# Kernel optimization log

Measured on AMD Instinct MI355X. Metric: run time of the kernel, lower is better.

Reference implementation:

```python
import jax, jax.numpy as jnp
import numpy as np
import math

N, E, B, T = 100000, 500000, 4096, 12
IN, HID, H = 64, 32, 4
HC = HID * H  # 128
ED = 4


def setup_inputs() -> dict:
    key = jax.random.key(0)
    ks = jax.random.split(key, 40)
    w = lambda k, shape: jax.random.normal(k, shape, jnp.float32) * 0.05
    inp = {
        'x': jax.random.normal(ks[0], (N, IN), jnp.float32),
        'edge_index': jax.random.randint(ks[1], (2, E), 0, N, jnp.int32),
        'edge_attr': jax.random.normal(ks[2], (E, ED), jnp.float32),
        'batch': jnp.sort(jax.random.randint(ks[3], (N,), 0, B, jnp.int32)),
        'r_target': jax.random.randint(ks[4], (B,), 0, T, jnp.int32),
        # layer 1 (in=IN)
        'Wq1': w(ks[5], (IN, HC)), 'bq1': w(ks[6], (HC,)),
        'Wk1': w(ks[7], (IN, HC)), 'bk1': w(ks[8], (HC,)),
        'Wv1': w(ks[9], (IN, HC)), 'bv1': w(ks[10], (HC,)),
        'We1': w(ks[11], (ED, HC)),
        'Ws1': w(ks[12], (IN, HC)), 'bs1': w(ks[13], (HC,)),
        # layers 2 and 3 stacked (in=HC)
        'Wq23': w(ks[14], (2, HC, HC)), 'bq23': w(ks[15], (2, HC)),
        'Wk23': w(ks[16], (2, HC, HC)), 'bk23': w(ks[17], (2, HC)),
        'Wv23': w(ks[18], (2, HC, HC)), 'bv23': w(ks[19], (2, HC)),
        'We23': w(ks[20], (2, ED, HC)),
        'Ws23': w(ks[21], (2, HC, HC)), 'bs23': w(ks[22], (2, HC)),
        # per-task linear heads (out_channels=1)
        'head_W': w(ks[23], (T, HC)), 'head_b': w(ks[24], (T,)),
    }
    return inp


def tconv(x, src, dst, ea, Wq, bq, Wk, bk, Wv, bv, We, Ws, bs):
    """PyG TransformerConv: gather -> per-edge MHA score -> segment softmax -> scatter."""
    q = (x @ Wq + bq).reshape(-1, H, HID)   # [N,H,C]
    k = (x @ Wk + bk).reshape(-1, H, HID)
    v = (x @ Wv + bv).reshape(-1, H, HID)
    e = (ea @ We).reshape(-1, H, HID)       # [E,H,C] (lin_edge has no bias)
    kj = k[src] + e                          # [E,H,C]
    alpha = (q[dst] * kj).sum(-1) / math.sqrt(HID)          # [E,H]
    amax = jax.ops.segment_max(alpha, dst, num_segments=N)  # [N,H]
    alpha = jnp.exp(alpha - amax[dst])
    asum = jax.ops.segment_sum(alpha, dst, num_segments=N)
    alpha = alpha / (asum[dst] + 1e-16)
    msg = (v[src] + e) * alpha[..., None]                   # [E,H,C]
    out = jax.ops.segment_sum(msg, dst, num_segments=N).reshape(N, HC)
    return out + x @ Ws + bs                 # root_weight skip connection


def reference(x, edge_index, edge_attr, batch, r_target,
              Wq1, bq1, Wk1, bk1, Wv1, bv1, We1, Ws1, bs1,
              Wq23, bq23, Wk23, bk23, Wv23, bv23, We23, Ws23, bs23,
              head_W, head_b):
    src, dst = edge_index[0], edge_index[1]
    h = jax.nn.relu(tconv(x, src, dst, edge_attr, Wq1, bq1, Wk1, bk1, Wv1, bv1, We1, Ws1, bs1))
    h = jax.nn.relu(tconv(h, src, dst, edge_attr, Wq23[0], bq23[0], Wk23[0], bk23[0], Wv23[0], bv23[0], We23[0], Ws23[0], bs23[0]))
    h = tconv(h, src, dst, edge_attr, Wq23[1], bq23[1], Wk23[1], bk23[1], Wv23[1], bv23[1], We23[1], Ws23[1], bs23[1])
    # global mean pool per graph
    cnt = jax.ops.segment_sum(jnp.ones((N,), h.dtype), batch, num_segments=B)
    pooled = jax.ops.segment_sum(h, batch, num_segments=B) / jnp.maximum(cnt, 1.0)[:, None]  # [B,HC]
    # dropout p=0.3 is a no-op in eval mode
    # per-task head selected by r_target (out_channels=1, squeezed)
    return (pooled * head_W[r_target]).sum(-1) + head_b[r_target]  # [B]
```

## Files before the change

kernel.cpp:

```cpp
#include <hip/hip_runtime.h>
#include <hip/hip_bf16.h>

#define NN 100000
#define EE 500000
#define BB 4096
#define HC 128
#define SCAN_ELEM 1024
#define NSB ((NN + SCAN_ELEM - 1) / SCAN_ELEM)

typedef __bf16 bf16_t;
typedef bf16_t bf16x8 __attribute__((ext_vector_type(8)));
typedef float f32x4 __attribute__((ext_vector_type(4)));

__device__ __forceinline__ unsigned short f2bf(float f) {
    unsigned u = __builtin_bit_cast(unsigned, f);
    u += 0x7FFFu + ((u >> 16) & 1u);
    return (unsigned short)(u >> 16);
}
__device__ __forceinline__ float bflo(unsigned u) {
    return __builtin_bit_cast(float, u << 16);
}
__device__ __forceinline__ float bfhi(unsigned u) {
    return __builtin_bit_cast(float, u & 0xFFFF0000u);
}

__global__ __launch_bounds__(256) void conv_x(const float* __restrict__ in,
                                              unsigned short* __restrict__ outb,
                                              int total4)
{
    const int g = blockIdx.x * 256 + threadIdx.x;
    if (g >= total4) return;
    const float4 f = *(const float4*)(in + (size_t)g * 4);
    ushort4 u;
    u.x = f2bf(f.x); u.y = f2bf(f.y); u.z = f2bf(f.z); u.w = f2bf(f.w);
    *(ushort4*)(outb + (size_t)g * 4) = u;
}

__global__ __launch_bounds__(256) void prep_w(
    const float* __restrict__ Wq, const float* __restrict__ Wk,
    const float* __restrict__ Wv, const float* __restrict__ Ws,
    unsigned short* __restrict__ Wt, int K)
{
    const int g = blockIdx.x * 256 + threadIdx.x;
    const int per = K * 128;
    if (g >= 4 * per) return;
    const int p = g / per, r = g - p * per;
    const int k = r >> 7, n = r & 127;
    const float* W = p == 0 ? Wq : p == 1 ? Wk : p == 2 ? Wv : Ws;
    Wt[(size_t)p * per + (size_t)n * K + k] = f2bf(W[k * 128 + n]);
}

template<int NKT>
__global__ __launch_bounds__(256) void gemm_mfma(
    const unsigned short* __restrict__ A,
    const unsigned short* __restrict__ Wt,
    const float* __restrict__ bq, const float* __restrict__ bk,
    const float* __restrict__ bv, const float* __restrict__ bs,
    unsigned* __restrict__ Qb, unsigned* __restrict__ Kb,
    unsigned* __restrict__ Vb, float* __restrict__ S)
{
    constexpr int K = NKT * 32;
    const int lane = threadIdx.x & 63;
    const int p = threadIdx.x >> 6;
    const int m = lane & 15, kq = lane >> 4;
    const int rows0 = blockIdx.x * 32;

    const unsigned short* Wp = Wt + (size_t)p * 128 * K;
    const float* bias = p == 0 ? bq : p == 1 ? bk : p == 2 ? bv : bs;

    bf16x8 a[2][NKT];
#pragma unroll
    for (int mt = 0; mt < 2; mt++)
#pragma unroll
        for (int kt = 0; kt < NKT; kt++)
            a[mt][kt] = *(const bf16x8*)(A + (size_t)(rows0 + mt * 16 + m) * K + kt * 32 + kq * 8);

    f32x4 acc[2][8];
#pragma unroll
    for (int mt = 0; mt < 2; mt++)
#pragma unroll
        for (int nt = 0; nt < 8; nt++)
            acc[mt][nt] = (f32x4){0.f, 0.f, 0.f, 0.f};

#pragma unroll
    for (int nt = 0; nt < 8; nt++) {
#pragma unroll
        for (int kt = 0; kt < NKT; kt++) {
            const bf16x8 b = *(const bf16x8*)(Wp + (size_t)(nt * 16 + m) * K + kt * 32 + kq * 8);
            acc[0][nt] = __builtin_amdgcn_mfma_f32_16x16x32_bf16(a[0][kt], b, acc[0][nt], 0, 0, 0);
            acc[1][nt] = __builtin_amdgcn_mfma_f32_16x16x32_bf16(a[1][kt], b, acc[1][nt], 0, 0, 0);
        }
    }

    if (p == 3) {
#pragma unroll
        for (int nt = 0; nt < 8; nt++) {
            const float bi = bias[nt * 16 + m];
#pragma unroll
            for (int mt = 0; mt < 2; mt++) {
                float* o = S + (size_t)(rows0 + mt * 16 + kq * 4) * HC + nt * 16 + m;
#pragma unroll
                for (int r = 0; r < 4; r++) o[r * HC] = acc[mt][nt][r] + bi;
            }
        }
    } else {
        unsigned* out = p == 0 ? Qb : p == 1 ? Kb : Vb;
#pragma unroll
        for (int nt = 0; nt < 8; nt++) {
            const float bi = bias[nt * 16 + m];
#pragma unroll
            for (int mt = 0; mt < 2; mt++) {
#pragma unroll
                for (int r = 0; r < 4; r++) {
                    const float v0 = acc[mt][nt][r] + bi;
                    const float v1 = __shfl_xor(v0, 1);
                    if (!(m & 1)) {
                        const unsigned pk = (unsigned)f2bf(v0) | ((unsigned)f2bf(v1) << 16);
                        out[(size_t)(rows0 + mt * 16 + kq * 4 + r) * 64 + nt * 8 + (m >> 1)] = pk;
                    }
                }
            }
        }
    }
}

__global__ __launch_bounds__(256) void deg_k(const int* __restrict__ ei, int* __restrict__ deg)
{
    const int e = blockIdx.x * 256 + threadIdx.x;
    if (e < EE) atomicAdd(&deg[ei[EE + e]], 1);
}

__global__ __launch_bounds__(256) void scan_part(const int* __restrict__ deg,
                                                 int* __restrict__ bsum)
{
    __shared__ int red[256];
    const int base = blockIdx.x * SCAN_ELEM + threadIdx.x * 4;
    int s = 0;
#pragma unroll
    for (int j = 0; j < 4; j++) { const int i = base + j; if (i < NN) s += deg[i]; }
    red[threadIdx.x] = s;
    __syncthreads();
    for (int st = 128; st > 0; st >>= 1) {
        if (threadIdx.x < st) red[threadIdx.x] += red[threadIdx.x + st];
        __syncthreads();
    }
    if (threadIdx.x == 0) bsum[blockIdx.x] = red[0];
}

__global__ __launch_bounds__(128) void scan_top(const int* __restrict__ bsum,
                                                int* __restrict__ boff)
{
    __shared__ int buf[128];
    const int v = (threadIdx.x < NSB) ? bsum[threadIdx.x] : 0;
    buf[threadIdx.x] = v;
    __syncthreads();
    for (int s = 1; s < 128; s <<= 1) {
        const int t = (threadIdx.x >= s) ? buf[threadIdx.x - s] : 0;
        __syncthreads();
        buf[threadIdx.x] += t;
        __syncthreads();
    }
    if (threadIdx.x < NSB) boff[threadIdx.x] = buf[threadIdx.x] - v;
}

__global__ __launch_bounds__(256) void scan_final(const int* __restrict__ deg,
                                                  const int* __restrict__ boff,
                                                  int* __restrict__ off,
                                                  int* __restrict__ cursor)
{
    __shared__ int tsum[256];
    const int base = blockIdx.x * SCAN_ELEM + threadIdx.x * 4;
    int vals[4];
    int s = 0;
#pragma unroll
    for (int j = 0; j < 4; j++) {
        const int i = base + j;
        vals[j] = (i < NN) ? deg[i] : 0;
        s += vals[j];
    }
    tsum[threadIdx.x] = s;
    __syncthreads();
    for (int st = 1; st < 256; st <<= 1) {
        const int t = (threadIdx.x >= st) ? tsum[threadIdx.x - st] : 0;
        __syncthreads();
        tsum[threadIdx.x] += t;
        __syncthreads();
    }
    int ex = boff[blockIdx.x] + tsum[threadIdx.x] - s;
#pragma unroll
    for (int j = 0; j < 4; j++) {
        const int i = base + j;
        if (i < NN) { off[i] = ex; cursor[i] = ex; }
        ex += vals[j];
    }
    if (blockIdx.x == NSB - 1 && threadIdx.x == 255)
        off[NN] = boff[blockIdx.x] + tsum[255];
}

__global__ __launch_bounds__(256) void bucket_k(const int* __restrict__ ei,
                                                const float* __restrict__ ea,
                                                int* __restrict__ cursor,
                                                int* __restrict__ esrc,
                                                float4* __restrict__ eaf)
{
    const int e = blockIdx.x * 256 + threadIdx.x;
    if (e < EE) {
        const int d = ei[EE + e];
        const int p = atomicAdd(&cursor[d], 1);
        esrc[p] = ei[e];
        eaf[p] = *(const float4*)(ea + (size_t)e * 4);
    }
}

__global__ __launch_bounds__(256) void cnt_k(const int* __restrict__ batch,
                                             float* __restrict__ cnt)
{
    const int n = blockIdx.x * 256 + threadIdx.x;
    if (n < NN) atomicAdd(&cnt[batch[n]], 1.0f);
}

__global__ __launch_bounds__(256) void edge_fused(
    const int* __restrict__ esrc, const float4* __restrict__ eaf,
    const float* __restrict__ We,
    const unsigned* __restrict__ Qb, const unsigned* __restrict__ Kb,
    const unsigned* __restrict__ Vb,
    const int* __restrict__ off, const float* __restrict__ S,
    unsigned short* __restrict__ Hb,
    const int* __restrict__ batch, float* __restrict__ pooled,
    int fuse_pool)
{
    __shared__ float wes[512];
    for (int i = threadIdx.x; i < 512; i += 256) wes[i] = We[i];
    __syncthreads();

    const int lane = threadIdx.x & 63;
    const int n = blockIdx.x * 4 + (threadIdx.x >> 6);
    const int c = lane * 2;
    const float w00 = wes[c],     w10 = wes[128 + c],     w20 = wes[256 + c],     w30 = wes[384 + c];
    const float w01 = wes[c + 1], w11 = wes[128 + c + 1], w21 = wes[256 + c + 1], w31 = wes[384 + c + 1];

    const int beg = off[n], end = off[n + 1];
    const unsigned qu = Qb[(size_t)n * 64 + lane];
    const float q0 = bflo(qu), q1 = bfhi(qu);
    float num0 = 0.f, num1 = 0.f, den = 0.f;

    int src = 0;
    float4 a4 = make_float4(0.f, 0.f, 0.f, 0.f);
    if (beg < end) { src = esrc[beg]; a4 = eaf[beg]; }

    for (int p = beg; p < end; p++) {
        const unsigned ku = Kb[(size_t)src * 64 + lane];
        const unsigned vu = Vb[(size_t)src * 64 + lane];
        const float4 ac = a4;
        if (p + 1 < end) { src = esrc[p + 1]; a4 = eaf[p + 1]; }
        const float e0 = ac.x * w00 + ac.y * w10 + ac.z * w20 + ac.w * w30;
        const float e1 = ac.x * w01 + ac.y * w11 + ac.z * w21 + ac.w * w31;
        float part = q0 * (bflo(ku) + e0) + q1 * (bfhi(ku) + e1);
        part += __shfl_xor(part, 1);
        part += __shfl_xor(part, 2);
        part += __shfl_xor(part, 4);
        part += __shfl_xor(part, 8);
        const float al = expf(part * 0.17677669529663687f);
        num0 += (bflo(vu) + e0) * al;
        num1 += (bfhi(vu) + e1) * al;
        den += al;
    }

    const float2 skip = *(const float2*)(S + (size_t)n * HC + c);
    const float inv = 1.f / (den + 1e-16f);
    float o0 = num0 * inv + skip.x;
    float o1 = num1 * inv + skip.y;
    if (!fuse_pool) {
        o0 = fmaxf(o0, 0.f);
        o1 = fmaxf(o1, 0.f);
        const unsigned pk = (unsigned)f2bf(o0) | ((unsigned)f2bf(o1) << 16);
        *(unsigned*)(Hb + (size_t)n * HC + c) = pk;
    } else {
        const int b = batch[n];
        atomicAdd(pooled + (size_t)b * HC + c, o0);
        atomicAdd(pooled + (size_t)b * HC + c + 1, o1);
    }
}

__global__ __launch_bounds__(256) void head_k(
    const float* __restrict__ pooled, const float* __restrict__ cnt,
    const int* __restrict__ rt, const float* __restrict__ hW,
    const float* __restrict__ hb, float* __restrict__ out)
{
    const int lane = threadIdx.x & 63;
    const int b = blockIdx.x * 4 + (threadIdx.x >> 6);
    if (b >= BB) return;
    const int t = rt[b];
    const int c = lane * 2;
    const float2 p2 = *(const float2*)(pooled + (size_t)b * HC + c);
    const float2 w2 = *(const float2*)(hW + (size_t)t * HC + c);
    float part = p2.x * w2.x + p2.y * w2.y;
    part += __shfl_xor(part, 1);
    part += __shfl_xor(part, 2);
    part += __shfl_xor(part, 4);
    part += __shfl_xor(part, 8);
    part += __shfl_xor(part, 16);
    part += __shfl_xor(part, 32);
    if (lane == 0) out[b] = part / fmaxf(cnt[b], 1.0f) + hb[t];
}

extern "C" void kernel_launch(void* const* d_in, const int* in_sizes, int n_in,
                              void* d_out, int out_size, void* d_ws, size_t ws_size,
                              hipStream_t stream) {
    const float* x      = (const float*)d_in[0];
    const int*   ei     = (const int*)d_in[1];
    const float* ea     = (const float*)d_in[2];
    const int*   batch  = (const int*)d_in[3];
    const int*   rt     = (const int*)d_in[4];

    float* ws     = (float*)d_ws;
    float* Hbuf   = ws;
    unsigned* Qb  = (unsigned*)(ws + 12800000);
    unsigned* Kb  = Qb + 6400000;
    unsigned* Vb  = Kb + 6400000;
    unsigned short* Abf = (unsigned short*)(Vb + 6400000);
    float4* eaf   = (float4*)(Abf + 12800000);
    unsigned short* Wt = (unsigned short*)(eaf + 500000);
    float* pooled = (float*)(Wt + 65536);
    float* cnt    = pooled + 524288;
    int*   esrc   = (int*)(cnt + 4096);
    int*   deg    = esrc + 500000;
    int*   off    = deg + 100000;
    int*   cursor = off + 100004;
    int*   bsum   = cursor + 100000;
    int*   boff   = bsum + 128;

    hipMemsetAsync(deg, 0, 100000 * sizeof(int), stream);
    deg_k<<<(EE + 255) / 256, 256, 0, stream>>>(ei, deg);
    scan_part<<<NSB, 256, 0, stream>>>(deg, bsum);
    scan_top<<<1, 128, 0, stream>>>(bsum, boff);
    scan_final<<<NSB, 256, 0, stream>>>(deg, boff, off, cursor);
    bucket_k<<<(EE + 255) / 256, 256, 0, stream>>>(ei, ea, cursor, esrc, eaf);

    hipMemsetAsync(pooled, 0, (size_t)(BB * HC + BB) * sizeof(float), stream);
    cnt_k<<<(NN + 255) / 256, 256, 0, stream>>>(batch, cnt);

    conv_x<<<(NN * 64 / 4 + 255) / 256, 256, 0, stream>>>(x, Abf, NN * 64 / 4);

    for (int l = 0; l < 3; l++) {
        const int K = (l == 0) ? 64 : 128;
        const float *Wq, *Wk, *Wv, *Wsk, *bq, *bk, *bv, *bs, *We;
        if (l == 0) {
            Wq = (const float*)d_in[5];  bq = (const float*)d_in[6];
            Wk = (const float*)d_in[7];  bk = (const float*)d_in[8];
            Wv = (const float*)d_in[9];  bv = (const float*)d_in[10];
            We = (const float*)d_in[11];
            Wsk= (const float*)d_in[12]; bs = (const float*)d_in[13];
        } else {
            const int j = l - 1;
            Wq = (const float*)d_in[14] + (size_t)j * HC * HC;  bq = (const float*)d_in[15] + j * HC;
            Wk = (const float*)d_in[16] + (size_t)j * HC * HC;  bk = (const float*)d_in[17] + j * HC;
            Wv = (const float*)d_in[18] + (size_t)j * HC * HC;  bv = (const float*)d_in[19] + j * HC;
            We = (const float*)d_in[20] + (size_t)j * 4 * HC;
            Wsk= (const float*)d_in[21] + (size_t)j * HC * HC;  bs = (const float*)d_in[22] + j * HC;
        }

        prep_w<<<(4 * K * 128 + 255) / 256, 256, 0, stream>>>(Wq, Wk, Wv, Wsk, Wt, K);
        if (K == 64)
            gemm_mfma<2><<<NN / 32, 256, 0, stream>>>(Abf, Wt, bq, bk, bv, bs, Qb, Kb, Vb, Hbuf);
        else
            gemm_mfma<4><<<NN / 32, 256, 0, stream>>>(Abf, Wt, bq, bk, bv, bs, Qb, Kb, Vb, Hbuf);
        edge_fused<<<NN / 4, 256, 0, stream>>>(esrc, eaf, We, Qb, Kb, Vb, off,
                                               Hbuf, Abf, batch, pooled,
                                               l == 2 ? 1 : 0);
    }

    head_k<<<BB / 4, 256, 0, stream>>>(pooled, cnt, rt,
        (const float*)d_in[23], (const float*)d_in[24], (float*)d_out);
}
```

Baseline: 665.9 us.

## Process four edges per wavefront in parallel with 16-byte feature loads

New measurement: 653.9 us. About the same (-1.8%).

```diff
diff --git a/kernel.cpp b/kernel.cpp
--- a/kernel.cpp
+++ b/kernel.cpp
@@ -229,56 +229,107 @@
     const int* __restrict__ batch, float* __restrict__ pooled,
     int fuse_pool)
 {
-    __shared__ float wes[512];
-    for (int i = threadIdx.x; i < 512; i += 256) wes[i] = We[i];
-    __syncthreads();
-
     const int lane = threadIdx.x & 63;
+    const int slot = lane >> 4;
+    const int c8   = lane & 15;
     const int n = blockIdx.x * 4 + (threadIdx.x >> 6);
-    const int c = lane * 2;
-    const float w00 = wes[c],     w10 = wes[128 + c],     w20 = wes[256 + c],     w30 = wes[384 + c];
-    const float w01 = wes[c + 1], w11 = wes[128 + c + 1], w21 = wes[256 + c + 1], w31 = wes[384 + c + 1];
+
+    float w[4][8];
+#pragma unroll
+    for (int d = 0; d < 4; d++) {
+        const float4 a = *(const float4*)(We + d * HC + c8 * 8);
+        const float4 b = *(const float4*)(We + d * HC + c8 * 8 + 4);
+        w[d][0] = a.x; w[d][1] = a.y; w[d][2] = a.z; w[d][3] = a.w;
+        w[d][4] = b.x; w[d][5] = b.y; w[d][6] = b.z; w[d][7] = b.w;
+    }
+
+    const uint4 qv = *(const uint4*)(Qb + (size_t)n * 64 + c8 * 4);
+    float q[8];
+    q[0] = bflo(qv.x); q[1] = bfhi(qv.x); q[2] = bflo(qv.y); q[3] = bfhi(qv.y);
+    q[4] = bflo(qv.z); q[5] = bfhi(qv.z); q[6] = bflo(qv.w); q[7] = bfhi(qv.w);
 
     const int beg = off[n], end = off[n + 1];
-    const unsigned qu = Qb[(size_t)n * 64 + lane];
-    const float q0 = bflo(qu), q1 = bfhi(qu);
-    float num0 = 0.f, num1 = 0.f, den = 0.f;
-
-    int src = 0;
-    float4 a4 = make_float4(0.f, 0.f, 0.f, 0.f);
-    if (beg < end) { src = esrc[beg]; a4 = eaf[beg]; }
-
-    for (int p = beg; p < end; p++) {
-        const unsigned ku = Kb[(size_t)src * 64 + lane];
-        const unsigned vu = Vb[(size_t)src * 64 + lane];
-        const float4 ac = a4;
-        if (p + 1 < end) { src = esrc[p + 1]; a4 = eaf[p + 1]; }
-        const float e0 = ac.x * w00 + ac.y * w10 + ac.z * w20 + ac.w * w30;
-        const float e1 = ac.x * w01 + ac.y * w11 + ac.z * w21 + ac.w * w31;
-        float part = q0 * (bflo(ku) + e0) + q1 * (bfhi(ku) + e1);
-        part += __shfl_xor(part, 1);
-        part += __shfl_xor(part, 2);
-        part += __shfl_xor(part, 4);
-        part += __shfl_xor(part, 8);
-        const float al = expf(part * 0.17677669529663687f);
-        num0 += (bflo(vu) + e0) * al;
-        num1 += (bfhi(vu) + e1) * al;
-        den += al;
-    }
-
-    const float2 skip = *(const float2*)(S + (size_t)n * HC + c);
+    float num[8] = {0.f, 0.f, 0.f, 0.f, 0.f, 0.f, 0.f, 0.f};
+    float den = 0.f;
+
+    if (beg < end) {
+        int p0 = beg + slot; if (p0 >= end) p0 = end - 1;
+        int src = esrc[p0];
+        float4 a4 = eaf[p0];
+        for (int base = beg; base < end; base += 4) {
+            const bool act = (base + slot) < end;
+            const uint4 ku = *(const uint4*)(Kb + (size_t)src * 64 + c8 * 4);
+            const uint4 vu = *(const uint4*)(Vb + (size_t)src * 64 + c8 * 4);
+            const float4 ac = a4;
+            if (base + 4 < end) {
+                int pn = base + 4 + slot; if (pn >= end) pn = end - 1;
+                src = esrc[pn];
+                a4 = eaf[pn];
+            }
+            float e[8];
+#pragma unroll
+            for (int j = 0; j < 8; j++)
+                e[j] = ac.x * w[0][j] + ac.y * w[1][j] + ac.z * w[2][j] + ac.w * w[3][j];
+            float part = q[0] * (bflo(ku.x) + e[0]) + q[1] * (bfhi(ku.x) + e[1])
+                       + q[2] * (bflo(ku.y) + e[2]) + q[3] * (bfhi(ku.y) + e[3])
+                       + q[4] * (bflo(ku.z) + e[4]) + q[5] * (bfhi(ku.z) + e[5])
+                       + q[6] * (bflo(ku.w) + e[6]) + q[7] * (bfhi(ku.w) + e[7]);
+            part += __shfl_xor(part, 1);
+            part += __shfl_xor(part, 2);
+            float al = __expf(part * 0.17677669529663687f);
+            if (!act) al = 0.f;
+            num[0] += (bflo(vu.x) + e[0]) * al;
+            num[1] += (bfhi(vu.x) + e[1]) * al;
+            num[2] += (bflo(vu.y) + e[2]) * al;
+            num[3] += (bfhi(vu.y) + e[3]) * al;
+            num[4] += (bflo(vu.z) + e[4]) * al;
+            num[5] += (bfhi(vu.z) + e[5]) * al;
+            num[6] += (bflo(vu.w) + e[6]) * al;
+            num[7] += (bfhi(vu.w) + e[7]) * al;
+            den += al;
+        }
+    }
+
+#pragma unroll
+    for (int j = 0; j < 8; j++) {
+        num[j] += __shfl_xor(num[j], 16);
+        num[j] += __shfl_xor(num[j], 32);
+    }
+    den += __shfl_xor(den, 16);
+    den += __shfl_xor(den, 32);
     const float inv = 1.f / (den + 1e-16f);
-    float o0 = num0 * inv + skip.x;
-    float o1 = num1 * inv + skip.y;
+
     if (!fuse_pool) {
-        o0 = fmaxf(o0, 0.f);
-        o1 = fmaxf(o1, 0.f);
-        const unsigned pk = (unsigned)f2bf(o0) | ((unsigned)f2bf(o1) << 16);
-        *(unsigned*)(Hb + (size_t)n * HC + c) = pk;
+        if (slot == 0) {
+            const float4 s0 = *(const float4*)(S + (size_t)n * HC + c8 * 8);
+            const float4 s1 = *(const float4*)(S + (size_t)n * HC + c8 * 8 + 4);
+            float o[8];
+            o[0] = fmaxf(num[0] * inv + s0.x, 0.f);
+            o[1] = fmaxf(num[1] * inv + s0.y, 0.f);
+            o[2] = fmaxf(num[2] * inv + s0.z, 0.f);
+            o[3] = fmaxf(num[3] * inv + s0.w, 0.f);
+            o[4] = fmaxf(num[4] * inv + s1.x, 0.f);
+            o[5] = fmaxf(num[5] * inv + s1.y, 0.f);
+            o[6] = fmaxf(num[6] * inv + s1.z, 0.f);
+            o[7] = fmaxf(num[7] * inv + s1.w, 0.f);
+            uint4 pk;
+            pk.x = (unsigned)f2bf(o[0]) | ((unsigned)f2bf(o[1]) << 16);
+            pk.y = (unsigned)f2bf(o[2]) | ((unsigned)f2bf(o[3]) << 16);
+            pk.z = (unsigned)f2bf(o[4]) | ((unsigned)f2bf(o[5]) << 16);
+            pk.w = (unsigned)f2bf(o[6]) | ((unsigned)f2bf(o[7]) << 16);
+            *(uint4*)(Hb + (size_t)n * HC + c8 * 8) = pk;
+        }
     } else {
+        float oe, oo;
+        if      (slot == 0) { oe = num[0]; oo = num[1]; }
+        else if (slot == 1) { oe = num[2]; oo = num[3]; }
+        else if (slot == 2) { oe = num[4]; oo = num[5]; }
+        else                { oe = num[6]; oo = num[7]; }
+        const int c = c8 * 8 + slot * 2;
+        const float2 s2 = *(const float2*)(S + (size_t)n * HC + c);
         const int b = batch[n];
-        atomicAdd(pooled + (size_t)b * HC + c, o0);
-        atomicAdd(pooled + (size_t)b * HC + c + 1, o1);
+        atomicAdd(pooled + (size_t)b * HC + c,     oe * inv + s2.x);
+        atomicAdd(pooled + (size_t)b * HC + c + 1, oo * inv + s2.y);
     }
 }
 
```

## Process four edges per wave with interleaved K/V rows and factored edge terms

Applied to the files above, without the earlier changes.

Result: no change. 670.3 us (+0.7%).

```diff
diff --git a/kernel.cpp b/kernel.cpp
--- a/kernel.cpp
+++ b/kernel.cpp
@@ -11,6 +11,7 @@
 typedef __bf16 bf16_t;
 typedef bf16_t bf16x8 __attribute__((ext_vector_type(8)));
 typedef float f32x4 __attribute__((ext_vector_type(4)));
+typedef float f32x2 __attribute__((ext_vector_type(2)));
 
 __device__ __forceinline__ unsigned short f2bf(float f) {
     unsigned u = __builtin_bit_cast(unsigned, f);
@@ -22,6 +23,9 @@
 }
 __device__ __forceinline__ float bfhi(unsigned u) {
     return __builtin_bit_cast(float, u & 0xFFFF0000u);
+}
+__device__ __forceinline__ f32x2 unpk2(unsigned u) {
+    return (f32x2){ bflo(u), bfhi(u) };
 }
 
 __global__ __launch_bounds__(256) void conv_x(const float* __restrict__ in,
@@ -56,8 +60,8 @@
     const unsigned short* __restrict__ Wt,
     const float* __restrict__ bq, const float* __restrict__ bk,
     const float* __restrict__ bv, const float* __restrict__ bs,
-    unsigned* __restrict__ Qb, unsigned* __restrict__ Kb,
-    unsigned* __restrict__ Vb, float* __restrict__ S)
+    unsigned* __restrict__ Qb, unsigned* __restrict__ KVb,
+    float* __restrict__ S)
 {
     constexpr int K = NKT * 32;
     const int lane = threadIdx.x & 63;
@@ -104,7 +108,8 @@
             }
         }
     } else {
-        unsigned* out = p == 0 ? Qb : p == 1 ? Kb : Vb;
+        unsigned* out = p == 0 ? Qb : (p == 1 ? KVb : KVb + 64);
+        const int stride = p == 0 ? 64 : 128;
 #pragma unroll
         for (int nt = 0; nt < 8; nt++) {
             const float bi = bias[nt * 16 + m];
@@ -116,7 +121,7 @@
                     const float v1 = __shfl_xor(v0, 1);
                     if (!(m & 1)) {
                         const unsigned pk = (unsigned)f2bf(v0) | ((unsigned)f2bf(v1) << 16);
-                        out[(size_t)(rows0 + mt * 16 + kq * 4 + r) * 64 + nt * 8 + (m >> 1)] = pk;
+                        out[(size_t)(rows0 + mt * 16 + kq * 4 + r) * stride + nt * 8 + (m >> 1)] = pk;
                     }
                 }
             }
@@ -222,63 +227,135 @@
 __global__ __launch_bounds__(256) void edge_fused(
     const int* __restrict__ esrc, const float4* __restrict__ eaf,
     const float* __restrict__ We,
-    const unsigned* __restrict__ Qb, const unsigned* __restrict__ Kb,
-    const unsigned* __restrict__ Vb,
+    const unsigned* __restrict__ Qb, const unsigned* __restrict__ KVb,
     const int* __restrict__ off, const float* __restrict__ S,
     unsigned short* __restrict__ Hb,
     const int* __restrict__ batch, float* __restrict__ pooled,
     int fuse_pool)
 {
-    __shared__ float wes[512];
-    for (int i = threadIdx.x; i < 512; i += 256) wes[i] = We[i];
-    __syncthreads();
-
     const int lane = threadIdx.x & 63;
+    const int slot = lane >> 4;
+    const int c8   = lane & 15;
+    const int cb   = c8 * 8;
+    const int ceq  = cb + slot * 2;
     const int n = blockIdx.x * 4 + (threadIdx.x >> 6);
-    const int c = lane * 2;
-    const float w00 = wes[c],     w10 = wes[128 + c],     w20 = wes[256 + c],     w30 = wes[384 + c];
-    const float w01 = wes[c + 1], w11 = wes[128 + c + 1], w21 = wes[256 + c + 1], w31 = wes[384 + c + 1];
 
     const int beg = off[n], end = off[n + 1];
-    const unsigned qu = Qb[(size_t)n * 64 + lane];
-    const float q0 = bflo(qu), q1 = bfhi(qu);
-    float num0 = 0.f, num1 = 0.f, den = 0.f;
-
-    int src = 0;
-    float4 a4 = make_float4(0.f, 0.f, 0.f, 0.f);
-    if (beg < end) { src = esrc[beg]; a4 = eaf[beg]; }
-
-    for (int p = beg; p < end; p++) {
-        const unsigned ku = Kb[(size_t)src * 64 + lane];
-        const unsigned vu = Vb[(size_t)src * 64 + lane];
-        const float4 ac = a4;
-        if (p + 1 < end) { src = esrc[p + 1]; a4 = eaf[p + 1]; }
-        const float e0 = ac.x * w00 + ac.y * w10 + ac.z * w20 + ac.w * w30;
-        const float e1 = ac.x * w01 + ac.y * w11 + ac.z * w21 + ac.w * w31;
-        float part = q0 * (bflo(ku) + e0) + q1 * (bfhi(ku) + e1);
-        part += __shfl_xor(part, 1);
-        part += __shfl_xor(part, 2);
-        part += __shfl_xor(part, 4);
-        part += __shfl_xor(part, 8);
-        const float al = expf(part * 0.17677669529663687f);
-        num0 += (bflo(vu) + e0) * al;
-        num1 += (bfhi(vu) + e1) * al;
+
+    const float2 sk2 = *(const float2*)(S + (size_t)n * HC + ceq);
+    const uint4 qv = *(const uint4*)(Qb + (size_t)n * 64 + c8 * 4);
+    f32x2 q2[4];
+    q2[0] = unpk2(qv.x); q2[1] = unpk2(qv.y);
+    q2[2] = unpk2(qv.z); q2[3] = unpk2(qv.w);
+
+    float qep[4];
+#pragma unroll
+    for (int d = 0; d < 4; d++) {
+        const float4 wa = *(const float4*)(We + d * HC + cb);
+        const float4 wb = *(const float4*)(We + d * HC + cb + 4);
+        qep[d] = wa.x * q2[0].x + wa.y * q2[0].y + wa.z * q2[1].x + wa.w * q2[1].y
+               + wb.x * q2[2].x + wb.y * q2[2].y + wb.z * q2[3].x + wb.w * q2[3].y;
+    }
+
+    f32x2 num2[4] = {(f32x2){0.f, 0.f}, (f32x2){0.f, 0.f},
+                     (f32x2){0.f, 0.f}, (f32x2){0.f, 0.f}};
+    f32x4 s4 = (f32x4){0.f, 0.f, 0.f, 0.f};
+    float den = 0.f;
+
+    auto COMPUTE = [&](const uint4& ku, const uint4& vu, const float4& ac, bool act) {
+        f32x2 t2 = q2[0] * unpk2(ku.x);
+        t2 += q2[1] * unpk2(ku.y);
+        t2 += q2[2] * unpk2(ku.z);
+        t2 += q2[3] * unpk2(ku.w);
+        float tot = t2.x + t2.y
+                  + ac.x * qep[0] + ac.y * qep[1] + ac.z * qep[2] + ac.w * qep[3];
+        tot += __shfl_xor(tot, 1);
+        tot += __shfl_xor(tot, 2);
+        float al = __expf(tot * 0.17677669529663687f);
+        if (!act) al = 0.f;
+        num2[0] += unpk2(vu.x) * al;
+        num2[1] += unpk2(vu.y) * al;
+        num2[2] += unpk2(vu.z) * al;
+        num2[3] += unpk2(vu.w) * al;
+        s4.x += ac.x * al; s4.y += ac.y * al;
+        s4.z += ac.z * al; s4.w += ac.w * al;
         den += al;
-    }
-
-    const float2 skip = *(const float2*)(S + (size_t)n * HC + c);
+    };
+
+    if (beg < end) {
+        const int e1 = end - 1;
+        int p0 = beg + slot; if (p0 > e1) p0 = e1;
+        const int srcA = esrc[p0];
+        const float4 aA = eaf[p0];
+        const unsigned* kvA = KVb + (size_t)srcA * 128 + c8 * 4;
+        const uint4 kA = *(const uint4*)kvA;
+        const uint4 vA = *(const uint4*)(kvA + 64);
+        if (beg + 4 < end) {
+            int p1 = beg + 4 + slot; if (p1 > e1) p1 = e1;
+            const int srcB = esrc[p1];
+            float4 aB = eaf[p1];
+            const unsigned* kvB = KVb + (size_t)srcB * 128 + c8 * 4;
+            uint4 kB = *(const uint4*)kvB;
+            uint4 vB = *(const uint4*)(kvB + 64);
+            COMPUTE(kA, vA, aA, true);
+            int base = beg + 4;
+            for (;;) {
+                if (base + 4 < end) {
+                    int pn = base + 4 + slot; if (pn > e1) pn = e1;
+                    const int srcN = esrc[pn];
+                    const float4 aN = eaf[pn];
+                    COMPUTE(kB, vB, aB, (base + slot) < end);
+                    const unsigned* kvN = KVb + (size_t)srcN * 128 + c8 * 4;
+                    kB = *(const uint4*)kvN;
+                    vB = *(const uint4*)(kvN + 64);
+                    aB = aN;
+                    base += 4;
+                } else {
+                    COMPUTE(kB, vB, aB, (base + slot) < end);
+                    break;
+                }
+            }
+        } else {
+            COMPUTE(kA, vA, aA, (beg + slot) < end);
+        }
+    }
+
+#pragma unroll
+    for (int j = 0; j < 4; j++) {
+        num2[j].x += __shfl_xor(num2[j].x, 16);
+        num2[j].y += __shfl_xor(num2[j].y, 16);
+        num2[j].x += __shfl_xor(num2[j].x, 32);
+        num2[j].y += __shfl_xor(num2[j].y, 32);
+    }
+    s4.x += __shfl_xor(s4.x, 16); s4.y += __shfl_xor(s4.y, 16);
+    s4.z += __shfl_xor(s4.z, 16); s4.w += __shfl_xor(s4.w, 16);
+    s4.x += __shfl_xor(s4.x, 32); s4.y += __shfl_xor(s4.y, 32);
+    s4.z += __shfl_xor(s4.z, 32); s4.w += __shfl_xor(s4.w, 32);
+    den += __shfl_xor(den, 16);
+    den += __shfl_xor(den, 32);
     const float inv = 1.f / (den + 1e-16f);
-    float o0 = num0 * inv + skip.x;
-    float o1 = num1 * inv + skip.y;
+
+    f32x2 mynum = slot == 0 ? num2[0] : slot == 1 ? num2[1]
+                : slot == 2 ? num2[2] : num2[3];
+    float ev0 = 0.f, ev1 = 0.f;
+#pragma unroll
+    for (int d = 0; d < 4; d++) {
+        const float2 wd = *(const float2*)(We + d * HC + ceq);
+        const float sd = d == 0 ? s4.x : d == 1 ? s4.y : d == 2 ? s4.z : s4.w;
+        ev0 += sd * wd.x;
+        ev1 += sd * wd.y;
+    }
+    const float o0 = (mynum.x + ev0) * inv + sk2.x;
+    const float o1 = (mynum.y + ev1) * inv + sk2.y;
+
     if (!fuse_pool) {
-        o0 = fmaxf(o0, 0.f);
-        o1 = fmaxf(o1, 0.f);
-        const unsigned pk = (unsigned)f2bf(o0) | ((unsigned)f2bf(o1) << 16);
-        *(unsigned*)(Hb + (size_t)n * HC + c) = pk;
+        const float r0 = fmaxf(o0, 0.f), r1 = fmaxf(o1, 0.f);
+        const unsigned pk = (unsigned)f2bf(r0) | ((unsigned)f2bf(r1) << 16);
+        *(unsigned*)(Hb + (size_t)n * HC + ceq) = pk;
     } else {
         const int b = batch[n];
-        atomicAdd(pooled + (size_t)b * HC + c, o0);
-        atomicAdd(pooled + (size_t)b * HC + c + 1, o1);
+        atomicAdd(pooled + (size_t)b * HC + ceq,     o0);
+        atomicAdd(pooled + (size_t)b * HC + ceq + 1, o1);
     }
 }
 
@@ -316,9 +393,8 @@
     float* ws     = (float*)d_ws;
     float* Hbuf   = ws;
     unsigned* Qb  = (unsigned*)(ws + 12800000);
-    unsigned* Kb  = Qb + 6400000;
-    unsigned* Vb  = Kb + 6400000;
-    unsigned short* Abf = (unsigned short*)(Vb + 6400000);
+    unsigned* KVb = Qb + 6400000;
+    unsigned short* Abf = (unsigned short*)(KVb + 12800000);
     float4* eaf   = (float4*)(Abf + 12800000);
     unsigned short* Wt = (unsigned short*)(eaf + 500000);
     float* pooled = (float*)(Wt + 65536);
@@ -362,10 +438,10 @@
 
         prep_w<<<(4 * K * 128 + 255) / 256, 256, 0, stream>>>(Wq, Wk, Wv, Wsk, Wt, K);
         if (K == 64)
-            gemm_mfma<2><<<NN / 32, 256, 0, stream>>>(Abf, Wt, bq, bk, bv, bs, Qb, Kb, Vb, Hbuf);
+            gemm_mfma<2><<<NN / 32, 256, 0, stream>>>(Abf, Wt, bq, bk, bv, bs, Qb, KVb, Hbuf);
         else
-            gemm_mfma<4><<<NN / 32, 256, 0, stream>>>(Abf, Wt, bq, bk, bv, bs, Qb, Kb, Vb, Hbuf);
-        edge_fused<<<NN / 4, 256, 0, stream>>>(esrc, eaf, We, Qb, Kb, Vb, off,
+            gemm_mfma<4><<<NN / 32, 256, 0, stream>>>(Abf, Wt, bq, bk, bv, bs, Qb, KVb, Hbuf);
+        edge_fused<<<NN / 4, 256, 0, stream>>>(esrc, eaf, We, Qb, KVb, off,
                                                Hbuf, Abf, batch, pooled,
                                                l == 2 ? 1 : 0);
     }
```
